# Optimization experiments

Hardware: AMD Instinct MI355X
Metric: run time of the kernel (lower is better)

The kernel has to match this reference:

```python
import jax, jax.numpy as jnp
import numpy as np

IN, H1, H2, H3, H4, OUT = 512, 2048, 2048, 1024, 512, 1


def setup_inputs() -> dict:
    key = jax.random.key(0)
    ks = jax.random.split(key, 12)
    def lin(k, fan_in, fan_out):
        # torch Linear default init: U(-1/sqrt(fan_in), 1/sqrt(fan_in))
        bound = 1.0 / np.sqrt(fan_in)
        k1, k2 = jax.random.split(k)
        W = jax.random.uniform(k1, (fan_out, fan_in), jnp.float32, -bound, bound)
        b = jax.random.uniform(k2, (fan_out,), jnp.float32, -bound, bound)
        return W, b
    x = jax.random.normal(ks[0], (16384, IN), jnp.float32)
    cross_w = jnp.ones((IN,), jnp.float32)   # init.constant_(1.0)
    cross_b = jnp.zeros((IN,), jnp.float32)  # init.constant_(0.0)
    W1, b1 = lin(ks[1], IN, H1)
    W2, b2 = lin(ks[2], H1, H2)
    W3, b3 = lin(ks[3], H2, H3)
    W4, b4 = lin(ks[4], H3, H4)
    Wo, bo = lin(ks[5], H4, OUT)
    return {"x": x, "cross_w": cross_w, "cross_b": cross_b,
            "W1": W1, "b1": b1, "W2": W2, "b2": b2,
            "W3": W3, "b3": b3, "W4": W4, "b4": b4,
            "Wo": Wo, "bo": bo}


def reference(x, cross_w, cross_b, W1, b1, W2, b2, W3, b3, W4, b4, Wo, bo):
    # Cross layer: bmm(x0[...,None], x[...,None,:]) . w == x0 * (x . w)
    # (mathematically identical, avoids the O(f^2) outer product)
    xw = x @ cross_w                         # [B]
    h = x * xw[:, None] + cross_b + x        # [B, IN]
    h = jax.nn.relu(h @ W1.T + b1)           # [B, H1]
    h = jax.nn.relu(h @ W2.T + b2)           # [B, H2]
    h = jax.nn.relu(h @ W3.T + b3)           # [B, H3]
    h = jax.nn.relu(h @ W4.T + b4)           # [B, H4]
    return h @ Wo.T + bo                     # [B, OUT]
```

## Files before the change

### kernel.cpp

```cpp
#include <hip/hip_runtime.h>


#define BK 64

typedef __bf16 bf16x8 __attribute__((ext_vector_type(8)));
typedef float  f32x4  __attribute__((ext_vector_type(4)));
typedef unsigned short u16x4 __attribute__((ext_vector_type(4)));

__device__ __forceinline__ unsigned short f2bf(float f) {
    unsigned int u = __builtin_bit_cast(unsigned int, f);
    u += 0x7fffu + ((u >> 16) & 1u);
    return (unsigned short)(u >> 16);
}
__device__ __forceinline__ float bf2f(unsigned short h) {
    unsigned int u = ((unsigned int)h) << 16;
    return __builtin_bit_cast(float, u);
}

__device__ __forceinline__ void async16(const void* g, void* l) {
    __builtin_amdgcn_global_load_lds(
        (const __attribute__((address_space(1))) unsigned int*)g,
        (__attribute__((address_space(3))) unsigned int*)l,
        16, 0, 0);
}

template<int BN>
__global__ __launch_bounds__(256, 2)
void gemm_bt_bias_relu(const unsigned short* __restrict__ A,
                       const unsigned short* __restrict__ B,
                       const float* __restrict__ bias,
                       unsigned short* __restrict__ C,
                       int M, int N, int K)
{
    constexpr int JT = BN / 32;
    __shared__ __align__(16) unsigned short As[128 * BK];
    __shared__ __align__(16) unsigned short Bs[2 * BN * BK];

    const int tid  = threadIdx.x;
    const int lane = tid & 63;
    const int wave = tid >> 6;
    const int quad = lane >> 4;
    const int l16  = lane & 15;

    const int bm = blockIdx.x * 128;
    const int bn = blockIdx.y * BN;
    const int wm = (wave & 1) * 64;
    const int wn = (wave >> 1) * (BN / 2);

    const int lrow = tid >> 3;
    const int gcol = ((tid & 7) ^ (lrow & 7)) * 8;

    const unsigned short* gaBase = A + (size_t)(bm + lrow) * K + gcol;
    const unsigned short* gbBase = B + (size_t)(bn + lrow) * K + gcol;

    unsigned short* lA = As + tid * 8;

    const int xa = l16 & 7;
    const unsigned short* As_w = As + (wm + l16) * BK;
    const int c0 = (quad ^ xa) * 8;
    const int c1 = ((quad ^ 4) ^ xa) * 8;

    f32x4 acc[4][JT] = {};
    bf16x8 areg[4];

    auto compute = [&](const unsigned short* Bsb) {
        const unsigned short* Bw = Bsb + (wn + l16) * BK;
#pragma unroll
        for (int kk = 0; kk < 2; ++kk) {
            const int cs = kk ? c1 : c0;
            bf16x8 af[4], bfr[JT];
#pragma unroll
            for (int i = 0; i < 4; ++i)  af[i]  = *(const bf16x8*)(As_w + i * 16 * BK + cs);
#pragma unroll
            for (int j = 0; j < JT; ++j) bfr[j] = *(const bf16x8*)(Bw + j * 16 * BK + cs);
#pragma unroll
            for (int i = 0; i < 4; ++i)
#pragma unroll
                for (int j = 0; j < JT; ++j)
                    acc[i][j] = __builtin_amdgcn_mfma_f32_16x16x32_bf16(
                        af[i], bfr[j], acc[i][j], 0, 0, 0);
        }
    };

    const int nk = K / BK;

#pragma unroll
    for (int i = 0; i < 4; ++i)
        areg[i] = *(const bf16x8*)(gaBase + (size_t)(i * 32) * K);
    {
        unsigned short* lB0 = Bs + tid * 8;
#pragma unroll
        for (int i = 0; i < JT; ++i)
            async16(gbBase + (size_t)(i * 32) * K, lB0 + i * 2048);
    }
#pragma unroll
    for (int i = 0; i < 4; ++i)
        *(bf16x8*)(lA + i * 2048) = areg[i];
    __syncthreads();

    for (int k = 0; k < nk - 1; ++k) {
        const size_t k0n = (size_t)(k + 1) * BK;
#pragma unroll
        for (int i = 0; i < 4; ++i)
            areg[i] = *(const bf16x8*)(gaBase + (size_t)(i * 32) * K + k0n);
        unsigned short* lBn = Bs + ((k + 1) & 1) * (BN * BK) + tid * 8;
#pragma unroll
        for (int i = 0; i < JT; ++i)
            async16(gbBase + (size_t)(i * 32) * K + k0n, lBn + i * 2048);

        compute(Bs + (k & 1) * (BN * BK));
        __syncthreads();
#pragma unroll
        for (int i = 0; i < 4; ++i)
            *(bf16x8*)(lA + i * 2048) = areg[i];
        __syncthreads();
    }
    compute(Bs + ((nk - 1) & 1) * (BN * BK));

    float bv[JT];
#pragma unroll
    for (int j = 0; j < JT; ++j) bv[j] = bias[bn + wn + j * 16 + l16];

#pragma unroll
    for (int i = 0; i < 4; ++i) {
        const int row0 = bm + wm + i * 16 + quad * 4;
#pragma unroll
        for (int j = 0; j < JT; ++j) {
            const int col = bn + wn + j * 16 + l16;
#pragma unroll
            for (int r = 0; r < 4; ++r) {
                float v = acc[i][j][r] + bv[j];
                v = fmaxf(v, 0.0f);
                C[(size_t)(row0 + r) * N + col] = f2bf(v);
            }
        }
    }
}

__global__ __launch_bounds__(256)
void prep_kernel(const float* __restrict__ x, const float* __restrict__ cw,
                 const float* __restrict__ cb, unsigned short* __restrict__ h0,
                 const float* __restrict__ s1, const float* __restrict__ s2,
                 const float* __restrict__ s3, const float* __restrict__ s4,
                 unsigned short* __restrict__ d1, unsigned short* __restrict__ d2,
                 unsigned short* __restrict__ d3, unsigned short* __restrict__ d4)
{
    const int b = blockIdx.x;
    if (b < 7680) {
        long t = (long)b * 256 + threadIdx.x;
        const float* s; unsigned short* d; long off;
        if (t < 262144L)       { s = s1; d = d1; off = t; }
        else if (t < 1310720L) { s = s2; d = d2; off = t - 262144L; }
        else if (t < 1835008L) { s = s3; d = d3; off = t - 1310720L; }
        else                   { s = s4; d = d4; off = t - 1835008L; }
        f32x4 f = *(const f32x4*)(s + off * 4);
        u16x4 o;
#pragma unroll
        for (int i = 0; i < 4; ++i) o[i] = f2bf(f[i]);
        *(u16x4*)(d + off * 4) = o;
    } else {
        const int row  = (b - 7680) * 4 + (threadIdx.x >> 6);
        const int lane = threadIdx.x & 63;
        const float* xr = x + (size_t)row * 512;
        float xv[8];
        float s = 0.f;
#pragma unroll
        for (int i = 0; i < 8; ++i) {
            const int c = lane + i * 64;
            xv[i] = xr[c];
            s += xv[i] * cw[c];
        }
#pragma unroll
        for (int off = 32; off > 0; off >>= 1) s += __shfl_down(s, off, 64);
        s = __shfl(s, 0, 64);
        unsigned short* hr = h0 + (size_t)row * 512;
#pragma unroll
        for (int i = 0; i < 8; ++i) {
            const int c = lane + i * 64;
            hr[c] = f2bf(xv[i] * s + cb[c] + xv[i]);
        }
    }
}

__global__ __launch_bounds__(256)
void final_dot(const unsigned short* __restrict__ h4, const float* __restrict__ Wo,
               const float* __restrict__ bo, float* __restrict__ out)
{
    const int row  = blockIdx.x * 4 + (threadIdx.x >> 6);
    const int lane = threadIdx.x & 63;
    const unsigned short* hr = h4 + (size_t)row * 512;
    float s = 0.f;
#pragma unroll
    for (int i = 0; i < 8; ++i) {
        const int c = lane + i * 64;
        s += bf2f(hr[c]) * Wo[c];
    }
#pragma unroll
    for (int off = 32; off > 0; off >>= 1) s += __shfl_down(s, off, 64);
    if (lane == 0) out[row] = s + bo[0];
}

extern "C" void kernel_launch(void* const* d_in, const int* in_sizes, int n_in,
                              void* d_out, int out_size, void* d_ws, size_t ws_size,
                              hipStream_t stream)
{
    const float* x  = (const float*)d_in[0];
    const float* cw = (const float*)d_in[1];
    const float* cb = (const float*)d_in[2];
    const float* W1 = (const float*)d_in[3];  const float* b1 = (const float*)d_in[4];
    const float* W2 = (const float*)d_in[5];  const float* b2 = (const float*)d_in[6];
    const float* W3 = (const float*)d_in[7];  const float* b3 = (const float*)d_in[8];
    const float* W4 = (const float*)d_in[9];  const float* b4 = (const float*)d_in[10];
    const float* Wo = (const float*)d_in[11]; const float* bo = (const float*)d_in[12];
    float* out = (float*)d_out;

    char* p = (char*)d_ws;
    unsigned short* wb1 = (unsigned short*)p; p += (size_t)2048 * 512  * 2;
    unsigned short* wb2 = (unsigned short*)p; p += (size_t)2048 * 2048 * 2;
    unsigned short* wb3 = (unsigned short*)p; p += (size_t)1024 * 2048 * 2;
    unsigned short* wb4 = (unsigned short*)p; p += (size_t)512  * 1024 * 2;
    unsigned short* actA = (unsigned short*)p; p += (size_t)16384 * 2048 * 2;
    unsigned short* actB = (unsigned short*)p;

    prep_kernel<<<11776, 256, 0, stream>>>(x, cw, cb, actA,
                                           W1, W2, W3, W4, wb1, wb2, wb3, wb4);

    gemm_bt_bias_relu<256><<<dim3(128, 8), 256, 0, stream>>>(actA, wb1, b1, actB, 16384, 2048, 512);
    gemm_bt_bias_relu<256><<<dim3(128, 8), 256, 0, stream>>>(actB, wb2, b2, actA, 16384, 2048, 2048);
    gemm_bt_bias_relu<256><<<dim3(128, 4), 256, 0, stream>>>(actA, wb3, b3, actB, 16384, 1024, 2048);
    gemm_bt_bias_relu<128><<<dim3(128, 4), 256, 0, stream>>>(actB, wb4, b4, actA, 16384, 512, 1024);
    final_dot<<<4096, 256, 0, stream>>>(actA, Wo, bo, out);
}
```

Measured before the change: 375.5 us.

## Switch GEMM to 32x32x16 MFMA with single-buffered async LDS loads

Replaces the 16x16x32 MFMA tiling with 32x32x16 bf16 MFMA instructions, which need fewer LDS fragment reads per FLOP. The A tile is now loaded with direct global-to-LDS async copies instead of going through registers. B is single-buffered, so the software pipeline is dropped: each K step loads, syncs, computes, then syncs again. This saves registers and LDS but exposes global load latency on every step, because loads no longer overlap compute.

Result: no change. 382.9 us (+2.0%).

```diff
diff --git a/kernel.cpp b/kernel.cpp
--- a/kernel.cpp
+++ b/kernel.cpp
@@ -5,6 +5,7 @@
 
 typedef __bf16 bf16x8 __attribute__((ext_vector_type(8)));
 typedef float  f32x4  __attribute__((ext_vector_type(4)));
+typedef float  f32x16 __attribute__((ext_vector_type(16)));
 typedef unsigned short u16x4 __attribute__((ext_vector_type(4)));
 
 __device__ __forceinline__ unsigned short f2bf(float f) {
@@ -33,14 +34,16 @@
                        int M, int N, int K)
 {
     constexpr int JT = BN / 32;
+    constexpr int NT = BN / 64;
     __shared__ __align__(16) unsigned short As[128 * BK];
-    __shared__ __align__(16) unsigned short Bs[2 * BN * BK];
+    __shared__ __align__(16) unsigned short Bs[BN * BK];
 
     const int tid  = threadIdx.x;
     const int lane = tid & 63;
     const int wave = tid >> 6;
-    const int quad = lane >> 4;
-    const int l16  = lane & 15;
+    const int l31  = lane & 31;
+    const int kh   = lane >> 5;
+    const int xa   = lane & 7;
 
     const int bm = blockIdx.x * 128;
     const int bn = blockIdx.y * BN;
@@ -54,84 +57,56 @@
     const unsigned short* gbBase = B + (size_t)(bn + lrow) * K + gcol;
 
     unsigned short* lA = As + tid * 8;
-
-    const int xa = l16 & 7;
-    const unsigned short* As_w = As + (wm + l16) * BK;
-    const int c0 = (quad ^ xa) * 8;
-    const int c1 = ((quad ^ 4) ^ xa) * 8;
-
-    f32x4 acc[4][JT] = {};
-    bf16x8 areg[4];
-
-    auto compute = [&](const unsigned short* Bsb) {
-        const unsigned short* Bw = Bsb + (wn + l16) * BK;
-#pragma unroll
-        for (int kk = 0; kk < 2; ++kk) {
-            const int cs = kk ? c1 : c0;
-            bf16x8 af[4], bfr[JT];
-#pragma unroll
-            for (int i = 0; i < 4; ++i)  af[i]  = *(const bf16x8*)(As_w + i * 16 * BK + cs);
-#pragma unroll
-            for (int j = 0; j < JT; ++j) bfr[j] = *(const bf16x8*)(Bw + j * 16 * BK + cs);
-#pragma unroll
-            for (int i = 0; i < 4; ++i)
-#pragma unroll
-                for (int j = 0; j < JT; ++j)
-                    acc[i][j] = __builtin_amdgcn_mfma_f32_16x16x32_bf16(
+    unsigned short* lB = Bs + tid * 8;
+
+    const unsigned short* As_w = As + (wm + l31) * BK;
+    const unsigned short* Bs_w = Bs + (wn + l31) * BK;
+
+    f32x16 acc[2][NT] = {};
+
+    for (int k0 = 0; k0 < K; k0 += BK) {
+#pragma unroll
+        for (int i = 0; i < 4; ++i)
+            async16(gaBase + (size_t)(i * 32) * K + k0, lA + i * 2048);
+#pragma unroll
+        for (int i = 0; i < JT; ++i)
+            async16(gbBase + (size_t)(i * 32) * K + k0, lB + i * 2048);
+        __syncthreads();
+
+#pragma unroll
+        for (int s = 0; s < 4; ++s) {
+            const int cs = ((2 * s + kh) ^ xa) * 8;
+            bf16x8 af[2], bfr[NT];
+#pragma unroll
+            for (int i = 0; i < 2; ++i)  af[i]  = *(const bf16x8*)(As_w + i * 32 * BK + cs);
+#pragma unroll
+            for (int j = 0; j < NT; ++j) bfr[j] = *(const bf16x8*)(Bs_w + j * 32 * BK + cs);
+#pragma unroll
+            for (int i = 0; i < 2; ++i)
+#pragma unroll
+                for (int j = 0; j < NT; ++j)
+                    acc[i][j] = __builtin_amdgcn_mfma_f32_32x32x16_bf16(
                         af[i], bfr[j], acc[i][j], 0, 0, 0);
         }
-    };
-
-    const int nk = K / BK;
-
-#pragma unroll
-    for (int i = 0; i < 4; ++i)
-        areg[i] = *(const bf16x8*)(gaBase + (size_t)(i * 32) * K);
-    {
-        unsigned short* lB0 = Bs + tid * 8;
-#pragma unroll
-        for (int i = 0; i < JT; ++i)
-            async16(gbBase + (size_t)(i * 32) * K, lB0 + i * 2048);
-    }
-#pragma unroll
-    for (int i = 0; i < 4; ++i)
-        *(bf16x8*)(lA + i * 2048) = areg[i];
-    __syncthreads();
-
-    for (int k = 0; k < nk - 1; ++k) {
-        const size_t k0n = (size_t)(k + 1) * BK;
-#pragma unroll
-        for (int i = 0; i < 4; ++i)
-            areg[i] = *(const bf16x8*)(gaBase + (size_t)(i * 32) * K + k0n);
-        unsigned short* lBn = Bs + ((k + 1) & 1) * (BN * BK) + tid * 8;
-#pragma unroll
-        for (int i = 0; i < JT; ++i)
-            async16(gbBase + (size_t)(i * 32) * K + k0n, lBn + i * 2048);
-
-        compute(Bs + (k & 1) * (BN * BK));
         __syncthreads();
-#pragma unroll
-        for (int i = 0; i < 4; ++i)
-            *(bf16x8*)(lA + i * 2048) = areg[i];
-        __syncthreads();
-    }
-    compute(Bs + ((nk - 1) & 1) * (BN * BK));
-
-    float bv[JT];
-#pragma unroll
-    for (int j = 0; j < JT; ++j) bv[j] = bias[bn + wn + j * 16 + l16];
-
-#pragma unroll
-    for (int i = 0; i < 4; ++i) {
-        const int row0 = bm + wm + i * 16 + quad * 4;
-#pragma unroll
-        for (int j = 0; j < JT; ++j) {
-            const int col = bn + wn + j * 16 + l16;
-#pragma unroll
-            for (int r = 0; r < 4; ++r) {
+    }
+
+    float bv[NT];
+#pragma unroll
+    for (int j = 0; j < NT; ++j) bv[j] = bias[bn + wn + j * 32 + l31];
+
+#pragma unroll
+    for (int i = 0; i < 2; ++i) {
+        const int rbase = bm + wm + i * 32 + 4 * kh;
+#pragma unroll
+        for (int j = 0; j < NT; ++j) {
+            const int col = bn + wn + j * 32 + l31;
+#pragma unroll
+            for (int r = 0; r < 16; ++r) {
+                const int row = rbase + (r & 3) + 8 * (r >> 2);
                 float v = acc[i][j][r] + bv[j];
                 v = fmaxf(v, 0.0f);
-                C[(size_t)(row0 + r) * N + col] = f2bf(v);
+                C[(size_t)row * N + col] = f2bf(v);
             }
         }
     }
```
